# Kernel optimization log

Measured on AMD Instinct MI355X. Metric: run time of the kernel, lower is better.

## Reference

```python
import jax, jax.numpy as jnp
import numpy as np

N, E, D, H, OUT = 50000, 640000, 128, 128, 32


def setup_inputs() -> dict:
    key = jax.random.key(0)
    ks = jax.random.split(key, 12)
    s = 0.02
    return {
        "x": jax.random.normal(ks[0], (N, D), dtype=jnp.float32),
        "edge_src": jax.random.randint(ks[1], (E,), 0, N),
        "edge_dst": jax.random.randint(ks[2], (E,), 0, N),
        "Wp": jax.random.normal(ks[3], (D, H), dtype=jnp.float32) * s,
        "bp": jnp.zeros((H,), jnp.float32),
        "Wm": jax.random.normal(ks[4], (2 * H, H), dtype=jnp.float32) * s,
        "bm": jnp.zeros((H,), jnp.float32),
        "Wu": jax.random.normal(ks[5], (2 * H, H), dtype=jnp.float32) * s,
        "bu": jnp.zeros((H,), jnp.float32),
        "gamma": jnp.ones((H,), jnp.float32),
        "beta": jnp.zeros((H,), jnp.float32),
        "Wd": jax.random.normal(ks[6], (H, OUT), dtype=jnp.float32) * s,
        "bd": jnp.zeros((OUT,), jnp.float32),
    }


def reference(x, edge_src, edge_dst, Wp, bp, Wm, bm, Wu, bu, gamma, beta, Wd, bd):
    n = x.shape[0]
    h = H
    # node projection: [N, H]
    h0 = x @ Wp + bp
    # edge messages: relu(concat(h0[src], h0[dst]) @ Wm + bm), split matmul avoids concat
    msg = jax.nn.relu(h0[edge_src] @ Wm[:h] + h0[edge_dst] @ Wm[h:] + bm)  # [E, H]
    # segment-mean into target nodes
    pooled_sum = jax.ops.segment_sum(msg, edge_dst, num_segments=n)
    cnt = jax.ops.segment_sum(jnp.ones((msg.shape[0],), msg.dtype), edge_dst, num_segments=n)
    pooled = pooled_sum / jnp.maximum(cnt, 1.0)[:, None]  # [N, H]
    # residual next-state: relu(h0 + Dense(concat(h0, pooled)))
    upd = h0 @ Wu[:h] + pooled @ Wu[h:] + bu
    hn = jax.nn.relu(h0 + upd)
    # layer norm over feature axis
    mu = jnp.mean(hn, axis=-1, keepdims=True)
    var = jnp.mean(jnp.square(hn - mu), axis=-1, keepdims=True)
    hn = (hn - mu) * jax.lax.rsqrt(var + 1e-6) * gamma + beta
    # graph-level mean pool -> [1, H] -> [1, OUT]
    g = jnp.mean(hn, axis=0, keepdims=True)
    return g @ Wd + bd
```

## Files before the change

### kernel.cpp

```cpp
#include <hip/hip_runtime.h>

#define N_NODES 50000
#define N_EDGES 640000
#define HD 128
#define TILE_N 128
#define NSCB 196
#define NTILE 391
#define HB 313

typedef short bf16x8 __attribute__((ext_vector_type(8)));
typedef float f32x4 __attribute__((ext_vector_type(4)));
typedef unsigned short u16x8 __attribute__((ext_vector_type(8)));
typedef unsigned short u16x4 __attribute__((ext_vector_type(4)));

__device__ __forceinline__ unsigned short f2bf(float f) {
  unsigned u = __float_as_uint(f);
  return (unsigned short)((u + 0x7fffu + ((u >> 16) & 1u)) >> 16);
}
__device__ __forceinline__ float bf2f(unsigned short h) {
  return __uint_as_float(((unsigned)h) << 16);
}
__device__ __forceinline__ int swzb(int row, int u) {
  return row * 256 + ((u ^ (row & 7)) << 4);
}

__device__ __forceinline__ void load_A(const char* Ash, int lane, int wr, bf16x8 A[4][4]) {
  const int l15 = lane & 15, l4 = lane >> 4;
#pragma unroll
  for (int rt = 0; rt < 4; ++rt)
#pragma unroll
    for (int kk = 0; kk < 4; ++kk)
      A[rt][kk] = *(const bf16x8*)(Ash + swzb(wr * 64 + rt * 16 + l15, kk * 4 + l4));
}

__device__ __forceinline__ void mfma_AB(const bf16x8 A[4][4], const char* Bsh,
                                        int lane, int wc, f32x4 acc[4][4]) {
  const int l15 = lane & 15, l4 = lane >> 4;
#pragma unroll
  for (int ct = 0; ct < 4; ++ct) {
    bf16x8 B[4];
#pragma unroll
    for (int kk = 0; kk < 4; ++kk)
      B[kk] = *(const bf16x8*)(Bsh + swzb(wc * 64 + ct * 16 + l15, kk * 4 + l4));
#pragma unroll
    for (int rt = 0; rt < 4; ++rt)
#pragma unroll
      for (int kk = 0; kk < 4; ++kk)
        acc[rt][ct] =
            __builtin_amdgcn_mfma_f32_16x16x32_bf16(A[rt][kk], B[kk], acc[rt][ct], 0, 0, 0);
  }
}

__device__ __forceinline__ void scatter_acc(char* Tsh, int lane, int wr, int wc,
                                            const f32x4 acc[4][4]) {
  const int l15 = lane & 15, l4 = lane >> 4;
#pragma unroll
  for (int rt = 0; rt < 4; ++rt)
#pragma unroll
    for (int ct = 0; ct < 4; ++ct) {
      int c = wc * 64 + ct * 16 + l15;
#pragma unroll
      for (int e = 0; e < 4; ++e) {
        int r = wr * 64 + rt * 16 + l4 * 4 + e;
        *(unsigned short*)(Tsh + swzb(r, c >> 3) + (c & 7) * 2) = f2bf(acc[rt][ct][e]);
      }
    }
}

__device__ __forceinline__ void copy_out(const char* Tsh, unsigned short* __restrict__ g,
                                         int bnode0, int tid) {
#pragma unroll
  for (int c = 0; c < 8; ++c) {
    int ul = c * 256 + tid;
    int row = ul >> 4, u = ul & 15;
    if (bnode0 + row < N_NODES)
      *(u16x8*)(g + (size_t)(bnode0 + row) * HD + u * 8) = *(const u16x8*)(Tsh + swzb(row, u));
  }
}

__device__ __forceinline__ void stage_bf(const unsigned short* __restrict__ src, char* Tsh,
                                         int bnode0, int tid, bool guard) {
#pragma unroll
  for (int c = 0; c < 8; ++c) {
    int ul = c * 256 + tid;
    int row = ul >> 4, u = ul & 15;
    u16x8 v = {0, 0, 0, 0, 0, 0, 0, 0};
    if (!guard || (bnode0 + row < N_NODES))
      v = *(const u16x8*)(src + (size_t)(bnode0 + row) * HD + u * 8);
    *(u16x8*)(Tsh + swzb(row, u)) = v;
  }
}

__device__ __forceinline__ void stage_xf(const float* __restrict__ src, char* Tsh,
                                         int bnode0, int tid) {
#pragma unroll
  for (int c = 0; c < 16; ++c) {
    int f4 = c * 256 + tid;
    int row = f4 >> 5, c4 = f4 & 31;
    float4 v = make_float4(0.f, 0.f, 0.f, 0.f);
    if (bnode0 + row < N_NODES) v = ((const float4*)src)[(size_t)(bnode0 + row) * 32 + c4];
    u16x4 p;
    p[0] = f2bf(v.x); p[1] = f2bf(v.y); p[2] = f2bf(v.z); p[3] = f2bf(v.w);
    *(u16x4*)(Tsh + swzb(row, c4 >> 1) + (c4 & 1) * 8) = p;
  }
}

__global__ __launch_bounds__(128) void k_prew(const float* __restrict__ Wp,
                                              const float* __restrict__ Wm,
                                              const float* __restrict__ Wu,
                                              unsigned short* __restrict__ WT,
                                              int* __restrict__ zbase) {
  if (blockIdx.x >= 5) {
    int idx = (blockIdx.x - 5) * 512 + threadIdx.x * 4;
    *(int4*)(zbase + idx) = make_int4(0, 0, 0, 0);
    return;
  }
  const int s = blockIdx.x;
  const float* src = (s == 0) ? Wp : (s == 1) ? Wm : (s == 2) ? (Wm + HD * HD)
                     : (s == 3) ? Wu : (Wu + HD * HD);
  const int n = threadIdx.x;
  unsigned short* dst = WT + (size_t)s * HD * HD + (size_t)n * HD;
  for (int kc = 0; kc < HD; kc += 8) {
    u16x8 p;
#pragma unroll
    for (int j = 0; j < 8; ++j) p[j] = f2bf(src[(size_t)(kc + j) * HD + n]);
    *(u16x8*)(dst + kc) = p;
  }
}

__global__ __launch_bounds__(256, 2) void k_projhist(
    const float* __restrict__ x, const unsigned short* __restrict__ WT,
    const float* __restrict__ bp, const float* __restrict__ bm,
    unsigned short* __restrict__ h0, unsigned short* __restrict__ a,
    unsigned short* __restrict__ b, const int* __restrict__ edst,
    int* __restrict__ deg, int* __restrict__ pos_e) {
  __shared__ char Ssh[32768];
  __shared__ char Wsh[32768];
  if (blockIdx.x < HB) {
    for (int e = blockIdx.x * 256 + threadIdx.x; e < N_EDGES; e += HB * 256)
      pos_e[e] = atomicAdd(&deg[edst[e]], 1);
    return;
  }
  const int tid = threadIdx.x, lane = tid & 63, wid = tid >> 6;
  const int wr = wid >> 1, wc = wid & 1, l15 = lane & 15;
  const int bnode0 = (blockIdx.x - HB) * TILE_N;

  stage_xf(x, Ssh, bnode0, tid);
  stage_bf(WT, Wsh, 0, tid, false);
  __syncthreads();

  bf16x8 A[4][4];
  f32x4 acc[4][4];
  load_A(Ssh, lane, wr, A);
#pragma unroll
  for (int ct = 0; ct < 4; ++ct) {
    float bv = bp[wc * 64 + ct * 16 + l15];
    f32x4 sv = {bv, bv, bv, bv};
#pragma unroll
    for (int rt = 0; rt < 4; ++rt) acc[rt][ct] = sv;
  }
  mfma_AB(A, Wsh, lane, wc, acc);
  __syncthreads();
  scatter_acc(Ssh, lane, wr, wc, acc);
  stage_bf(WT + 1 * HD * HD, Wsh, 0, tid, false);
  __syncthreads();
  copy_out(Ssh, h0, bnode0, tid);
  load_A(Ssh, lane, wr, A);
#pragma unroll
  for (int ct = 0; ct < 4; ++ct) {
    f32x4 z = {0.f, 0.f, 0.f, 0.f};
#pragma unroll
    for (int rt = 0; rt < 4; ++rt) acc[rt][ct] = z;
  }
  mfma_AB(A, Wsh, lane, wc, acc);
  __syncthreads();
  scatter_acc(Ssh, lane, wr, wc, acc);
  stage_bf(WT + 2 * HD * HD, Wsh, 0, tid, false);
  __syncthreads();
  copy_out(Ssh, a, bnode0, tid);
#pragma unroll
  for (int ct = 0; ct < 4; ++ct) {
    float bv = bm[wc * 64 + ct * 16 + l15];
    f32x4 sv = {bv, bv, bv, bv};
#pragma unroll
    for (int rt = 0; rt < 4; ++rt) acc[rt][ct] = sv;
  }
  mfma_AB(A, Wsh, lane, wc, acc);
  __syncthreads();
  scatter_acc(Ssh, lane, wr, wc, acc);
  __syncthreads();
  copy_out(Ssh, b, bnode0, tid);
}

__global__ __launch_bounds__(256) void k_scan12(const int* __restrict__ deg,
                                                int* __restrict__ bsum,
                                                int* __restrict__ boff,
                                                int* __restrict__ row_start,
                                                int* __restrict__ done2) {
  __shared__ int sh[256];
  __shared__ int amLast;
  int i = blockIdx.x * 256 + threadIdx.x;
  sh[threadIdx.x] = (i < N_NODES) ? deg[i] : 0;
  __syncthreads();
  for (int off = 128; off > 0; off >>= 1) {
    if (threadIdx.x < off) sh[threadIdx.x] += sh[threadIdx.x + off];
    __syncthreads();
  }
  if (threadIdx.x == 0) {
    bsum[blockIdx.x] = sh[0];
    __threadfence();
    amLast = (atomicAdd(done2, 1) == gridDim.x - 1) ? 1 : 0;
  }
  __syncthreads();
  if (amLast) {
    __threadfence();
    int t = threadIdx.x;
    int v = (t < NSCB) ? bsum[t] : 0;
    sh[t] = v;
    __syncthreads();
    for (int off = 1; off < 256; off <<= 1) {
      int add = (t >= off) ? sh[t - off] : 0;
      __syncthreads();
      sh[t] += add;
      __syncthreads();
    }
    if (t < NSCB) boff[t] = sh[t] - v;
    if (t == 255) row_start[N_NODES] = sh[255];
  }
}

__global__ __launch_bounds__(256) void k_scan3(const int* __restrict__ deg,
                                               const int* __restrict__ boff,
                                               int* __restrict__ row_start) {
  __shared__ int sh[256];
  int t = threadIdx.x;
  int i = blockIdx.x * 256 + t;
  int v = (i < N_NODES) ? deg[i] : 0;
  sh[t] = v;
  __syncthreads();
  for (int off = 1; off < 256; off <<= 1) {
    int add = (t >= off) ? sh[t - off] : 0;
    __syncthreads();
    sh[t] += add;
    __syncthreads();
  }
  if (i < N_NODES) row_start[i] = boff[blockIdx.x] + sh[t] - v;
}

__global__ void k_scatter(const int* __restrict__ src, const int* __restrict__ dst,
                          const int* __restrict__ pos_e, const int* __restrict__ row_start,
                          int* __restrict__ es) {
  int e = blockIdx.x * 256 + threadIdx.x;
  if (e < N_EDGES) {
    int d = dst[e];
    es[row_start[d] + pos_e[e]] = src[e];
  }
}

__global__ __launch_bounds__(256) void k_agg(const unsigned short* __restrict__ a,
                                             const unsigned short* __restrict__ b,
                                             const int* __restrict__ es,
                                             const int* __restrict__ row_start,
                                             unsigned short* __restrict__ pooled) {
  const int node = blockIdx.x * 4 + (threadIdx.x >> 6);
  const int lane = threadIdx.x & 63;
  const int s = row_start[node];
  const int e = row_start[node + 1];
  const unsigned bu = ((const unsigned*)(b + (size_t)node * HD))[lane];
  const float bx = bf2f((unsigned short)(bu & 0xffffu));
  const float by = bf2f((unsigned short)(bu >> 16));
  float ax = 0.f, ay = 0.f;
  int i = s;
  for (; i + 8 <= e; i += 8) {
    unsigned av[8];
#pragma unroll
    for (int j = 0; j < 8; ++j)
      av[j] = ((const unsigned*)(a + (size_t)es[i + j] * HD))[lane];
#pragma unroll
    for (int j = 0; j < 8; ++j) {
      ax += fmaxf(bf2f((unsigned short)(av[j] & 0xffffu)) + bx, 0.f);
      ay += fmaxf(bf2f((unsigned short)(av[j] >> 16)) + by, 0.f);
    }
  }
  for (; i + 4 <= e; i += 4) {
    unsigned av[4];
#pragma unroll
    for (int j = 0; j < 4; ++j)
      av[j] = ((const unsigned*)(a + (size_t)es[i + j] * HD))[lane];
#pragma unroll
    for (int j = 0; j < 4; ++j) {
      ax += fmaxf(bf2f((unsigned short)(av[j] & 0xffffu)) + bx, 0.f);
      ay += fmaxf(bf2f((unsigned short)(av[j] >> 16)) + by, 0.f);
    }
  }
  for (; i < e; ++i) {
    unsigned a0 = ((const unsigned*)(a + (size_t)es[i] * HD))[lane];
    ax += fmaxf(bf2f((unsigned short)(a0 & 0xffffu)) + bx, 0.f);
    ay += fmaxf(bf2f((unsigned short)(a0 >> 16)) + by, 0.f);
  }
  const float inv = 1.f / fmaxf((float)(e - s), 1.f);
  unsigned o = (unsigned)f2bf(ax * inv) | ((unsigned)f2bf(ay * inv) << 16);
  ((unsigned*)(pooled + (size_t)node * HD))[lane] = o;
}

__global__ __launch_bounds__(256, 2) void k_upd(
    const unsigned short* __restrict__ h0, const unsigned short* __restrict__ pooled,
    const unsigned short* __restrict__ WT, const float* __restrict__ bu,
    const float* __restrict__ gamma, const float* __restrict__ beta,
    const float* __restrict__ Wd, const float* __restrict__ bd,
    float* __restrict__ gsum, int* __restrict__ done, float* __restrict__ out) {
  __shared__ char Ssh[32768];
  __shared__ char Wsh[32768];
  __shared__ int lastflag;
  const int tid = threadIdx.x, lane = tid & 63, wid = tid >> 6;
  const int wr = wid >> 1, wc = wid & 1, l15 = lane & 15, l4 = lane >> 4;
  const int bnode0 = blockIdx.x * TILE_N;

  stage_bf(pooled, Ssh, bnode0, tid, true);
  stage_bf(WT + 4 * HD * HD, Wsh, 0, tid, false);
  __syncthreads();

  bf16x8 A[4][4];
  f32x4 acc[4][4];
  load_A(Ssh, lane, wr, A);
#pragma unroll
  for (int ct = 0; ct < 4; ++ct) {
    float bv = bu[wc * 64 + ct * 16 + l15];
    f32x4 sv = {bv, bv, bv, bv};
#pragma unroll
    for (int rt = 0; rt < 4; ++rt) acc[rt][ct] = sv;
  }
  mfma_AB(A, Wsh, lane, wc, acc);
  __syncthreads();
  stage_bf(h0, Ssh, bnode0, tid, true);
  stage_bf(WT + 3 * HD * HD, Wsh, 0, tid, false);
  __syncthreads();
  load_A(Ssh, lane, wr, A);
  mfma_AB(A, Wsh, lane, wc, acc);
  __syncthreads();

  float rsum[4][4], rsq[4][4];
#pragma unroll
  for (int rt = 0; rt < 4; ++rt)
#pragma unroll
    for (int e = 0; e < 4; ++e) {
      int r = wr * 64 + rt * 16 + l4 * 4 + e;
      float srow = 0.f, qrow = 0.f;
#pragma unroll
      for (int ct = 0; ct < 4; ++ct) {
        int c = wc * 64 + ct * 16 + l15;
        float hv = bf2f(*(const unsigned short*)(Ssh + swzb(r, c >> 3) + (c & 7) * 2));
        float v = fmaxf(hv + acc[rt][ct][e], 0.f);
        acc[rt][ct][e] = v;
        srow += v;
        qrow += v * v;
      }
#pragma unroll
      for (int m = 1; m < 16; m <<= 1) {
        srow += __shfl_xor(srow, m);
        qrow += __shfl_xor(qrow, m);
      }
      rsum[rt][e] = srow;
      rsq[rt][e] = qrow;
    }
  float* pS = (float*)Wsh;
  float* pQ = (float*)(Wsh + 1024);
  if (l15 == 0) {
#pragma unroll
    for (int rt = 0; rt < 4; ++rt)
#pragma unroll
      for (int e = 0; e < 4; ++e) {
        int r = wr * 64 + rt * 16 + l4 * 4 + e;
        pS[r * 2 + wc] = rsum[rt][e];
        pQ[r * 2 + wc] = rsq[rt][e];
      }
  }
  __syncthreads();

  float g4[4], b4[4];
#pragma unroll
  for (int ct = 0; ct < 4; ++ct) {
    int c = wc * 64 + ct * 16 + l15;
    g4[ct] = gamma[c];
    b4[ct] = beta[c];
  }
  float gp[4] = {0.f, 0.f, 0.f, 0.f};
#pragma unroll
  for (int rt = 0; rt < 4; ++rt)
#pragma unroll
    for (int e = 0; e < 4; ++e) {
      int r = wr * 64 + rt * 16 + l4 * 4 + e;
      float s = pS[r * 2] + pS[r * 2 + 1];
      float q = pQ[r * 2] + pQ[r * 2 + 1];
      float mu = s * (1.f / 128.f);
      float var = q * (1.f / 128.f) - mu * mu;
      float rs = rsqrtf(var + 1e-6f);
      bool valid = (bnode0 + r) < N_NODES;
#pragma unroll
      for (int ct = 0; ct < 4; ++ct) {
        float v = (acc[rt][ct][e] - mu) * rs * g4[ct] + b4[ct];
        if (valid) gp[ct] += v;
      }
    }
#pragma unroll
  for (int ct = 0; ct < 4; ++ct) {
    gp[ct] += __shfl_xor(gp[ct], 16);
    gp[ct] += __shfl_xor(gp[ct], 32);
  }
  if (lane < 16) {
#pragma unroll
    for (int ct = 0; ct < 4; ++ct) atomicAdd(&gsum[wc * 64 + ct * 16 + lane], gp[ct]);
  }

  __threadfence();
  __syncthreads();
  if (tid == 0) lastflag = (atomicAdd(done, 1) == gridDim.x - 1) ? 1 : 0;
  __syncthreads();
  if (lastflag) {
    __threadfence();
    if (tid < 32) {
      float acc2 = bd[tid];
      const float invN = 1.f / (float)N_NODES;
      for (int d = 0; d < HD; ++d) acc2 = fmaf(gsum[d] * invN, Wd[d * 32 + tid], acc2);
      out[tid] = acc2;
    }
  }
}

extern "C" void kernel_launch(void* const* d_in, const int* in_sizes, int n_in,
                              void* d_out, int out_size, void* d_ws, size_t ws_size,
                              hipStream_t stream) {
  (void)in_sizes; (void)n_in; (void)out_size; (void)ws_size;
  const float* x    = (const float*)d_in[0];
  const int* esrc   = (const int*)d_in[1];
  const int* edst   = (const int*)d_in[2];
  const float* Wp   = (const float*)d_in[3];
  const float* bp   = (const float*)d_in[4];
  const float* Wm   = (const float*)d_in[5];
  const float* bm   = (const float*)d_in[6];
  const float* Wu   = (const float*)d_in[7];
  const float* bu   = (const float*)d_in[8];
  const float* gam  = (const float*)d_in[9];
  const float* bet  = (const float*)d_in[10];
  const float* Wd   = (const float*)d_in[11];
  const float* bd   = (const float*)d_in[12];
  float* out = (float*)d_out;

  char* ws = (char*)d_ws;
  size_t off = 0;
  unsigned short* WT     = (unsigned short*)(ws + off); off += 5 * (size_t)HD * HD * 2;
  unsigned short* h0     = (unsigned short*)(ws + off); off += (size_t)N_NODES * HD * 2;
  unsigned short* a      = (unsigned short*)(ws + off); off += (size_t)N_NODES * HD * 2;
  unsigned short* b      = (unsigned short*)(ws + off); off += (size_t)N_NODES * HD * 2;
  unsigned short* pooled = (unsigned short*)(ws + off); off += (size_t)N_NODES * HD * 2;
  int* es    = (int*)(ws + off); off += (size_t)N_EDGES * 4;
  int* pos_e = (int*)(ws + off); off += (size_t)N_EDGES * 4;
  int* zbase = (int*)(ws + off);
  int* deg   = zbase;
  float* gsum = (float*)(zbase + N_NODES);
  int* done  = zbase + N_NODES + 128;
  int* done2 = zbase + N_NODES + 129;
  off += (size_t)50176 * 4;
  int* row_start = (int*)(ws + off); off += (size_t)(N_NODES + 1) * 4;
  int* bsum = (int*)(ws + off); off += (size_t)NSCB * 4;
  int* boff = (int*)(ws + off); off += (size_t)NSCB * 4;

  k_prew<<<103, 128, 0, stream>>>(Wp, Wm, Wu, WT, zbase);
  k_projhist<<<HB + NTILE, 256, 0, stream>>>(x, WT, bp, bm, h0, a, b, edst, deg, pos_e);
  k_scan12<<<NSCB, 256, 0, stream>>>(deg, bsum, boff, row_start, done2);
  k_scan3<<<NSCB, 256, 0, stream>>>(deg, boff, row_start);
  k_scatter<<<(N_EDGES + 255) / 256, 256, 0, stream>>>(esrc, edst, pos_e, row_start, es);
  k_agg<<<N_NODES / 4, 256, 0, stream>>>(a, b, es, row_start, pooled);
  k_upd<<<NTILE, 256, 0, stream>>>(h0, pooled, WT, bu, gam, bet, Wd, bd, gsum, done, out);
}
```

Measured before the change: 232.0 us.

## Read MFMA weights from global memory and merge scan kernels via spin flag

The projection and update kernels now read the B-operand weight fragments straight from global/L2 instead of staging them in a 32KB LDS buffer. Dropping that buffer lets the launch bounds rise to 3 and 4 blocks per CU and removes the staging passes and some barriers. The two scan kernels are also merged into one: the last block computes the block offsets and raises a flag, and every other block spin-waits on it. This saves a launch but depends on all 196 blocks being resident at once, and the weight loads now go through cache with less reuse.

Result: slower. 284.3 us (+22.6%).

```diff
diff --git a/kernel.cpp b/kernel.cpp
--- a/kernel.cpp
+++ b/kernel.cpp
@@ -33,15 +33,17 @@
       A[rt][kk] = *(const bf16x8*)(Ash + swzb(wr * 64 + rt * 16 + l15, kk * 4 + l4));
 }
 
-__device__ __forceinline__ void mfma_AB(const bf16x8 A[4][4], const char* Bsh,
-                                        int lane, int wc, f32x4 acc[4][4]) {
+__device__ __forceinline__ void mfma_ABg(const bf16x8 A[4][4],
+                                         const unsigned short* __restrict__ Wg,
+                                         int lane, int wc, f32x4 acc[4][4]) {
   const int l15 = lane & 15, l4 = lane >> 4;
 #pragma unroll
   for (int ct = 0; ct < 4; ++ct) {
+    const int row = wc * 64 + ct * 16 + l15;
     bf16x8 B[4];
 #pragma unroll
     for (int kk = 0; kk < 4; ++kk)
-      B[kk] = *(const bf16x8*)(Bsh + swzb(wc * 64 + ct * 16 + l15, kk * 4 + l4));
+      B[kk] = *(const bf16x8*)(Wg + (size_t)row * HD + (kk * 4 + l4) * 8);
 #pragma unroll
     for (int rt = 0; rt < 4; ++rt)
 #pragma unroll
@@ -128,14 +130,13 @@
   }
 }
 
-__global__ __launch_bounds__(256, 2) void k_projhist(
+__global__ __launch_bounds__(256, 3) void k_projhist(
     const float* __restrict__ x, const unsigned short* __restrict__ WT,
     const float* __restrict__ bp, const float* __restrict__ bm,
     unsigned short* __restrict__ h0, unsigned short* __restrict__ a,
     unsigned short* __restrict__ b, const int* __restrict__ edst,
     int* __restrict__ deg, int* __restrict__ pos_e) {
   __shared__ char Ssh[32768];
-  __shared__ char Wsh[32768];
   if (blockIdx.x < HB) {
     for (int e = blockIdx.x * 256 + threadIdx.x; e < N_EDGES; e += HB * 256)
       pos_e[e] = atomicAdd(&deg[edst[e]], 1);
@@ -146,7 +147,6 @@
   const int bnode0 = (blockIdx.x - HB) * TILE_N;
 
   stage_xf(x, Ssh, bnode0, tid);
-  stage_bf(WT, Wsh, 0, tid, false);
   __syncthreads();
 
   bf16x8 A[4][4];
@@ -159,10 +159,9 @@
 #pragma unroll
     for (int rt = 0; rt < 4; ++rt) acc[rt][ct] = sv;
   }
-  mfma_AB(A, Wsh, lane, wc, acc);
+  mfma_ABg(A, WT, lane, wc, acc);
   __syncthreads();
   scatter_acc(Ssh, lane, wr, wc, acc);
-  stage_bf(WT + 1 * HD * HD, Wsh, 0, tid, false);
   __syncthreads();
   copy_out(Ssh, h0, bnode0, tid);
   load_A(Ssh, lane, wr, A);
@@ -172,10 +171,9 @@
 #pragma unroll
     for (int rt = 0; rt < 4; ++rt) acc[rt][ct] = z;
   }
-  mfma_AB(A, Wsh, lane, wc, acc);
+  mfma_ABg(A, WT + 1 * HD * HD, lane, wc, acc);
   __syncthreads();
   scatter_acc(Ssh, lane, wr, wc, acc);
-  stage_bf(WT + 2 * HD * HD, Wsh, 0, tid, false);
   __syncthreads();
   copy_out(Ssh, a, bnode0, tid);
 #pragma unroll
@@ -185,56 +183,24 @@
 #pragma unroll
     for (int rt = 0; rt < 4; ++rt) acc[rt][ct] = sv;
   }
-  mfma_AB(A, Wsh, lane, wc, acc);
+  mfma_ABg(A, WT + 2 * HD * HD, lane, wc, acc);
   __syncthreads();
   scatter_acc(Ssh, lane, wr, wc, acc);
   __syncthreads();
   copy_out(Ssh, b, bnode0, tid);
 }
 
-__global__ __launch_bounds__(256) void k_scan12(const int* __restrict__ deg,
-                                                int* __restrict__ bsum,
-                                                int* __restrict__ boff,
-                                                int* __restrict__ row_start,
-                                                int* __restrict__ done2) {
+__global__ __launch_bounds__(256) void k_scan(const int* __restrict__ deg,
+                                              int* __restrict__ bsum,
+                                              int* __restrict__ boff,
+                                              int* __restrict__ row_start,
+                                              int* __restrict__ done2,
+                                              int* __restrict__ flag) {
   __shared__ int sh[256];
+  __shared__ int sh2[256];
   __shared__ int amLast;
-  int i = blockIdx.x * 256 + threadIdx.x;
-  sh[threadIdx.x] = (i < N_NODES) ? deg[i] : 0;
-  __syncthreads();
-  for (int off = 128; off > 0; off >>= 1) {
-    if (threadIdx.x < off) sh[threadIdx.x] += sh[threadIdx.x + off];
-    __syncthreads();
-  }
-  if (threadIdx.x == 0) {
-    bsum[blockIdx.x] = sh[0];
-    __threadfence();
-    amLast = (atomicAdd(done2, 1) == gridDim.x - 1) ? 1 : 0;
-  }
-  __syncthreads();
-  if (amLast) {
-    __threadfence();
-    int t = threadIdx.x;
-    int v = (t < NSCB) ? bsum[t] : 0;
-    sh[t] = v;
-    __syncthreads();
-    for (int off = 1; off < 256; off <<= 1) {
-      int add = (t >= off) ? sh[t - off] : 0;
-      __syncthreads();
-      sh[t] += add;
-      __syncthreads();
-    }
-    if (t < NSCB) boff[t] = sh[t] - v;
-    if (t == 255) row_start[N_NODES] = sh[255];
-  }
-}
-
-__global__ __launch_bounds__(256) void k_scan3(const int* __restrict__ deg,
-                                               const int* __restrict__ boff,
-                                               int* __restrict__ row_start) {
-  __shared__ int sh[256];
-  int t = threadIdx.x;
-  int i = blockIdx.x * 256 + t;
+  const int t = threadIdx.x;
+  const int i = blockIdx.x * 256 + t;
   int v = (i < N_NODES) ? deg[i] : 0;
   sh[t] = v;
   __syncthreads();
@@ -244,6 +210,32 @@
     sh[t] += add;
     __syncthreads();
   }
+  if (t == 0) {
+    bsum[blockIdx.x] = sh[255];
+    __threadfence();
+    amLast = (atomicAdd(done2, 1) == gridDim.x - 1) ? 1 : 0;
+  }
+  __syncthreads();
+  if (amLast) {
+    int bv = (t < NSCB) ? bsum[t] : 0;
+    sh2[t] = bv;
+    __syncthreads();
+    for (int off = 1; off < 256; off <<= 1) {
+      int add = (t >= off) ? sh2[t - off] : 0;
+      __syncthreads();
+      sh2[t] += add;
+      __syncthreads();
+    }
+    boff[t] = sh2[t] - bv;
+    if (t == 255) row_start[N_NODES] = sh2[255];
+    __threadfence();
+    __syncthreads();
+    if (t == 0) atomicExch(flag, 1);
+  }
+  if (t == 0) {
+    while (atomicAdd(flag, 0) == 0) __builtin_amdgcn_s_sleep(8);
+  }
+  __syncthreads();
   if (i < N_NODES) row_start[i] = boff[blockIdx.x] + sh[t] - v;
 }
 
@@ -303,21 +295,21 @@
   ((unsigned*)(pooled + (size_t)node * HD))[lane] = o;
 }
 
-__global__ __launch_bounds__(256, 2) void k_upd(
+__global__ __launch_bounds__(256, 4) void k_upd(
     const unsigned short* __restrict__ h0, const unsigned short* __restrict__ pooled,
     const unsigned short* __restrict__ WT, const float* __restrict__ bu,
     const float* __restrict__ gamma, const float* __restrict__ beta,
     const float* __restrict__ Wd, const float* __restrict__ bd,
     float* __restrict__ gsum, int* __restrict__ done, float* __restrict__ out) {
   __shared__ char Ssh[32768];
-  __shared__ char Wsh[32768];
+  __shared__ float pS[256];
+  __shared__ float pQ[256];
   __shared__ int lastflag;
   const int tid = threadIdx.x, lane = tid & 63, wid = tid >> 6;
   const int wr = wid >> 1, wc = wid & 1, l15 = lane & 15, l4 = lane >> 4;
   const int bnode0 = blockIdx.x * TILE_N;
 
   stage_bf(pooled, Ssh, bnode0, tid, true);
-  stage_bf(WT + 4 * HD * HD, Wsh, 0, tid, false);
   __syncthreads();
 
   bf16x8 A[4][4];
@@ -330,14 +322,12 @@
 #pragma unroll
     for (int rt = 0; rt < 4; ++rt) acc[rt][ct] = sv;
   }
-  mfma_AB(A, Wsh, lane, wc, acc);
+  mfma_ABg(A, WT + 4 * HD * HD, lane, wc, acc);
   __syncthreads();
   stage_bf(h0, Ssh, bnode0, tid, true);
-  stage_bf(WT + 3 * HD * HD, Wsh, 0, tid, false);
   __syncthreads();
   load_A(Ssh, lane, wr, A);
-  mfma_AB(A, Wsh, lane, wc, acc);
-  __syncthreads();
+  mfma_ABg(A, WT + 3 * HD * HD, lane, wc, acc);
 
   float rsum[4][4], rsq[4][4];
 #pragma unroll
@@ -363,8 +353,6 @@
       rsum[rt][e] = srow;
       rsq[rt][e] = qrow;
     }
-  float* pS = (float*)Wsh;
-  float* pQ = (float*)(Wsh + 1024);
   if (l15 == 0) {
 #pragma unroll
     for (int rt = 0; rt < 4; ++rt)
@@ -460,15 +448,15 @@
   float* gsum = (float*)(zbase + N_NODES);
   int* done  = zbase + N_NODES + 128;
   int* done2 = zbase + N_NODES + 129;
+  int* flag  = zbase + N_NODES + 130;
   off += (size_t)50176 * 4;
   int* row_start = (int*)(ws + off); off += (size_t)(N_NODES + 1) * 4;
-  int* bsum = (int*)(ws + off); off += (size_t)NSCB * 4;
-  int* boff = (int*)(ws + off); off += (size_t)NSCB * 4;
+  int* bsum = (int*)(ws + off); off += 256 * 4;
+  int* boff = (int*)(ws + off); off += 256 * 4;
 
   k_prew<<<103, 128, 0, stream>>>(Wp, Wm, Wu, WT, zbase);
   k_projhist<<<HB + NTILE, 256, 0, stream>>>(x, WT, bp, bm, h0, a, b, edst, deg, pos_e);
-  k_scan12<<<NSCB, 256, 0, stream>>>(deg, bsum, boff, row_start, done2);
-  k_scan3<<<NSCB, 256, 0, stream>>>(deg, boff, row_start);
+  k_scan<<<NSCB, 256, 0, stream>>>(deg, bsum, boff, row_start, done2, flag);
   k_scatter<<<(N_EDGES + 255) / 256, 256, 0, stream>>>(esrc, edst, pos_e, row_start, es);
   k_agg<<<N_NODES / 4, 256, 0, stream>>>(a, b, es, row_start, pooled);
   k_upd<<<NTILE, 256, 0, stream>>>(h0, pooled, WT, bu, gam, bet, Wd, bd, gsum, done, out);
```

## Fuse CSR histogram, scan and scatter into projection kernel with grid barriers

Applied to the files above, without the earlier changes.

The separate scan and scatter kernels are folded into the projection kernel. 256 dedicated blocks build the CSR: histogram, block scan, a top-level scan, then scatter, separated by spin-wait barriers on global atomic counters. The MFMA projection tiles run in parallel in the remaining blocks. This removes three kernel launches and lets CSR construction overlap the projection GEMMs. It relies on all 256 CSR blocks being co-resident, so a scheduling change could deadlock it.

New measurement: 304.7 us. +31.4%, slower.

```diff
diff --git a/kernel.cpp b/kernel.cpp
--- a/kernel.cpp
+++ b/kernel.cpp
@@ -4,9 +4,8 @@
 #define N_EDGES 640000
 #define HD 128
 #define TILE_N 128
-#define NSCB 196
 #define NTILE 391
-#define HB 313
+#define NCSR 256
 
 typedef short bf16x8 __attribute__((ext_vector_type(8)));
 typedef float f32x4 __attribute__((ext_vector_type(4)));
@@ -128,22 +127,88 @@
   }
 }
 
-__global__ __launch_bounds__(256, 2) void k_projhist(
+__global__ __launch_bounds__(256, 2) void k_mega(
     const float* __restrict__ x, const unsigned short* __restrict__ WT,
     const float* __restrict__ bp, const float* __restrict__ bm,
     unsigned short* __restrict__ h0, unsigned short* __restrict__ a,
-    unsigned short* __restrict__ b, const int* __restrict__ edst,
-    int* __restrict__ deg, int* __restrict__ pos_e) {
+    unsigned short* __restrict__ b, const int* __restrict__ esrc,
+    const int* __restrict__ edst, int* __restrict__ deg, int* __restrict__ pos_e,
+    int* __restrict__ es, int* __restrict__ row_start, int* __restrict__ bsum,
+    int* __restrict__ boff, int* __restrict__ ctrs) {
   __shared__ char Ssh[32768];
   __shared__ char Wsh[32768];
-  if (blockIdx.x < HB) {
-    for (int e = blockIdx.x * 256 + threadIdx.x; e < N_EDGES; e += HB * 256)
+  const int tid = threadIdx.x;
+
+  if (blockIdx.x < NCSR) {
+    int* done_h = ctrs + 0;
+    int* done_s = ctrs + 1;
+    int* flagS  = ctrs + 2;
+    int* done_r = ctrs + 3;
+    const int cb = blockIdx.x;
+    for (int e = cb * 256 + tid; e < N_EDGES; e += NCSR * 256)
       pos_e[e] = atomicAdd(&deg[edst[e]], 1);
+    __threadfence();
+    __syncthreads();
+    if (tid == 0) {
+      atomicAdd(done_h, 1);
+      while (atomicAdd(done_h, 0) < NCSR) __builtin_amdgcn_s_sleep(8);
+    }
+    __syncthreads();
+    int* sh = (int*)Ssh;
+    int* sh2 = (int*)(Ssh + 1024);
+    const int i = cb * 256 + tid;
+    int v = (i < N_NODES) ? deg[i] : 0;
+    sh[tid] = v;
+    __syncthreads();
+    for (int off = 1; off < 256; off <<= 1) {
+      int add = (tid >= off) ? sh[tid - off] : 0;
+      __syncthreads();
+      sh[tid] += add;
+      __syncthreads();
+    }
+    if (tid == 0) {
+      bsum[cb] = sh[255];
+      __threadfence();
+      atomicAdd(done_s, 1);
+    }
+    if (cb == 0) {
+      if (tid == 0)
+        while (atomicAdd(done_s, 0) < NCSR) __builtin_amdgcn_s_sleep(8);
+      __syncthreads();
+      int bv = bsum[tid];
+      sh2[tid] = bv;
+      __syncthreads();
+      for (int off = 1; off < 256; off <<= 1) {
+        int add = (tid >= off) ? sh2[tid - off] : 0;
+        __syncthreads();
+        sh2[tid] += add;
+        __syncthreads();
+      }
+      boff[tid] = sh2[tid] - bv;
+      if (tid == 255) row_start[N_NODES] = sh2[255];
+      __threadfence();
+      __syncthreads();
+      if (tid == 0) atomicExch(flagS, 1);
+    }
+    if (tid == 0)
+      while (atomicAdd(flagS, 0) == 0) __builtin_amdgcn_s_sleep(8);
+    __syncthreads();
+    if (i < N_NODES) row_start[i] = boff[cb] + sh[tid] - v;
+    __threadfence();
+    __syncthreads();
+    if (tid == 0) {
+      atomicAdd(done_r, 1);
+      while (atomicAdd(done_r, 0) < NCSR) __builtin_amdgcn_s_sleep(8);
+    }
+    __syncthreads();
+    for (int e = cb * 256 + tid; e < N_EDGES; e += NCSR * 256)
+      es[row_start[edst[e]] + pos_e[e]] = esrc[e];
     return;
   }
-  const int tid = threadIdx.x, lane = tid & 63, wid = tid >> 6;
+
+  const int lane = tid & 63, wid = tid >> 6;
   const int wr = wid >> 1, wc = wid & 1, l15 = lane & 15;
-  const int bnode0 = (blockIdx.x - HB) * TILE_N;
+  const int bnode0 = (blockIdx.x - NCSR) * TILE_N;
 
   stage_xf(x, Ssh, bnode0, tid);
   stage_bf(WT, Wsh, 0, tid, false);
@@ -190,71 +255,6 @@
   scatter_acc(Ssh, lane, wr, wc, acc);
   __syncthreads();
   copy_out(Ssh, b, bnode0, tid);
-}
-
-__global__ __launch_bounds__(256) void k_scan12(const int* __restrict__ deg,
-                                                int* __restrict__ bsum,
-                                                int* __restrict__ boff,
-                                                int* __restrict__ row_start,
-                                                int* __restrict__ done2) {
-  __shared__ int sh[256];
-  __shared__ int amLast;
-  int i = blockIdx.x * 256 + threadIdx.x;
-  sh[threadIdx.x] = (i < N_NODES) ? deg[i] : 0;
-  __syncthreads();
-  for (int off = 128; off > 0; off >>= 1) {
-    if (threadIdx.x < off) sh[threadIdx.x] += sh[threadIdx.x + off];
-    __syncthreads();
-  }
-  if (threadIdx.x == 0) {
-    bsum[blockIdx.x] = sh[0];
-    __threadfence();
-    amLast = (atomicAdd(done2, 1) == gridDim.x - 1) ? 1 : 0;
-  }
-  __syncthreads();
-  if (amLast) {
-    __threadfence();
-    int t = threadIdx.x;
-    int v = (t < NSCB) ? bsum[t] : 0;
-    sh[t] = v;
-    __syncthreads();
-    for (int off = 1; off < 256; off <<= 1) {
-      int add = (t >= off) ? sh[t - off] : 0;
-      __syncthreads();
-      sh[t] += add;
-      __syncthreads();
-    }
-    if (t < NSCB) boff[t] = sh[t] - v;
-    if (t == 255) row_start[N_NODES] = sh[255];
-  }
-}
-
-__global__ __launch_bounds__(256) void k_scan3(const int* __restrict__ deg,
-                                               const int* __restrict__ boff,
-                                               int* __restrict__ row_start) {
-  __shared__ int sh[256];
-  int t = threadIdx.x;
-  int i = blockIdx.x * 256 + t;
-  int v = (i < N_NODES) ? deg[i] : 0;
-  sh[t] = v;
-  __syncthreads();
-  for (int off = 1; off < 256; off <<= 1) {
-    int add = (t >= off) ? sh[t - off] : 0;
-    __syncthreads();
-    sh[t] += add;
-    __syncthreads();
-  }
-  if (i < N_NODES) row_start[i] = boff[blockIdx.x] + sh[t] - v;
-}
-
-__global__ void k_scatter(const int* __restrict__ src, const int* __restrict__ dst,
-                          const int* __restrict__ pos_e, const int* __restrict__ row_start,
-                          int* __restrict__ es) {
-  int e = blockIdx.x * 256 + threadIdx.x;
-  if (e < N_EDGES) {
-    int d = dst[e];
-    es[row_start[d] + pos_e[e]] = src[e];
-  }
 }
 
 __global__ __launch_bounds__(256) void k_agg(const unsigned short* __restrict__ a,
@@ -459,17 +459,15 @@
   int* deg   = zbase;
   float* gsum = (float*)(zbase + N_NODES);
   int* done  = zbase + N_NODES + 128;
-  int* done2 = zbase + N_NODES + 129;
+  int* ctrs  = zbase + N_NODES + 129;
   off += (size_t)50176 * 4;
   int* row_start = (int*)(ws + off); off += (size_t)(N_NODES + 1) * 4;
-  int* bsum = (int*)(ws + off); off += (size_t)NSCB * 4;
-  int* boff = (int*)(ws + off); off += (size_t)NSCB * 4;
+  int* bsum = (int*)(ws + off); off += 256 * 4;
+  int* boff = (int*)(ws + off); off += 256 * 4;
 
   k_prew<<<103, 128, 0, stream>>>(Wp, Wm, Wu, WT, zbase);
-  k_projhist<<<HB + NTILE, 256, 0, stream>>>(x, WT, bp, bm, h0, a, b, edst, deg, pos_e);
-  k_scan12<<<NSCB, 256, 0, stream>>>(deg, bsum, boff, row_start, done2);
-  k_scan3<<<NSCB, 256, 0, stream>>>(deg, boff, row_start);
-  k_scatter<<<(N_EDGES + 255) / 256, 256, 0, stream>>>(esrc, edst, pos_e, row_start, es);
+  k_mega<<<NCSR + NTILE, 256, 0, stream>>>(x, WT, bp, bm, h0, a, b, esrc, edst,
+                                           deg, pos_e, es, row_start, bsum, boff, ctrs);
   k_agg<<<N_NODES / 4, 256, 0, stream>>>(a, b, es, row_start, pooled);
   k_upd<<<NTILE, 256, 0, stream>>>(h0, pooled, WT, bu, gam, bet, Wd, bd, gsum, done, out);
 }
```
